# Kernel tuning notes

Measured on AMD Instinct MI355X. Metric: run time of the kernel, lower is better.

## Reference

```python
import jax, jax.numpy as jnp
import numpy as np

DT = 0.001
TAU_INV = 1.0 / 0.006   # tau_mem_inv == tau_syn_inv for both cells
V_TH = 1.0              # norse defaults: v_leak=0, v_reset=0


def heaviside(x):
    return (x > 0).astype(x.dtype)


def setup_inputs() -> dict:
    key = jax.random.key(0)
    k1, k2, k3 = jax.random.split(key, 3)
    T, B, I, H, O = 128, 2048, 64, 256, 16
    inp = jax.random.normal(k1, (T, B, I), dtype=jnp.float32)
    # torch.nn.Linear default init ~ U(-1/sqrt(fan_in), 1/sqrt(fan_in))
    w1 = jax.random.uniform(k2, (H, I), jnp.float32, -1.0, 1.0) / np.sqrt(I)
    w2 = jax.random.uniform(k3, (O, H), jnp.float32, -1.0, 1.0) / np.sqrt(H)
    return {"input": inp, "w1": w1, "w2": w2}


def _snn_forward(inp, w1, w2):
    B = inp.shape[1]
    H, O = w1.shape[0], w2.shape[0]
    decay = 1.0 - DT * TAU_INV

    def step(carry, x_t):
        v1, i1, v2, i2 = carry
        # LIF cell (hidden layer)
        g1 = x_t @ w1.T                              # [B, H]
        v_dec = v1 + DT * TAU_INV * (i1 - v1)        # Euler membrane update
        i_dec = i1 * decay                           # synaptic decay
        z = heaviside(v_dec - V_TH)                  # spikes
        v1n = (1.0 - z) * v_dec                      # reset to 0 where spiked
        i1n = i_dec + g1
        # LI cell (readout)
        g2 = z @ w2.T                                # [B, O]
        v2n = v2 + DT * TAU_INV * (i2 - v2)
        i2n = i2 * decay + g2
        return (v1n, i1n, v2n, i2n), (z, v2n)

    init = (jnp.zeros((B, H), inp.dtype), jnp.zeros((B, H), inp.dtype),
            jnp.zeros((B, O), inp.dtype), jnp.zeros((B, O), inp.dtype))
    _, (zs, ys) = jax.lax.scan(step, init, inp)
    score = jnp.max(ys, axis=0)                      # amax over time -> [B, O]
    spikes_mean = jnp.mean(jnp.sum(zs, axis=(0, 2)))
    return score, spikes_mean


def reference(input, w1, w2):
    return _snn_forward(input, w1, w2)
```

## Files before the change

kernel.cpp:

```cpp
#include <hip/hip_runtime.h>
#include <hip/hip_bf16.h>

#define T_STEPS 128
#define BATCH   2048
#define IN_F    64
#define HID     256
#define OUT_F   16
#define CH      8
#define NCH     (T_STEPS / CH)
#define SLAB    (BATCH * OUT_F)

typedef __attribute__((ext_vector_type(8))) short bf16x8;
typedef __attribute__((ext_vector_type(4))) float f32x4;
typedef unsigned short u16;
typedef unsigned int   u32;

__device__ __forceinline__ u16 f2bf(float f) {
    union { __hip_bfloat16 h; u16 u; } cv;
    cv.h = __float2bfloat16(f);
    return cv.u;
}
__device__ __forceinline__ float bf2f(u16 h) {
    return __uint_as_float(((u32)h) << 16);
}
__device__ __forceinline__ bf16x8 pack8(float4 a, float4 b) {
    bf16x8 r;
    r[0] = (short)f2bf(a.x); r[1] = (short)f2bf(a.y);
    r[2] = (short)f2bf(a.z); r[3] = (short)f2bf(a.w);
    r[4] = (short)f2bf(b.x); r[5] = (short)f2bf(b.y);
    r[6] = (short)f2bf(b.z); r[7] = (short)f2bf(b.w);
    return r;
}

__device__ __forceinline__ void lds_barrier() {
    __builtin_amdgcn_sched_barrier(0);
    asm volatile("s_waitcnt lgkmcnt(0)" ::: "memory");
    __builtin_amdgcn_sched_barrier(0);
    __builtin_amdgcn_s_barrier();
    __builtin_amdgcn_sched_barrier(0);
}

__global__ void snn_init_kernel(float* __restrict__ out) {
    if (threadIdx.x == 0 && blockIdx.x == 0) out[BATCH * OUT_F] = 0.0f;
}

__global__ void __launch_bounds__(512, 2)
snn_l1_kernel(const float* __restrict__ x, const float* __restrict__ w1,
              const float* __restrict__ w2, u16* __restrict__ g2p,
              float* __restrict__ out)
{
    const int tid  = threadIdx.x;
    const int lane = tid & 63;
    const int wv   = tid >> 6;
    const int hi   = lane >> 4;
    const int l15  = lane & 15;
    const int tile = blockIdx.x & 127;
    const int half = blockIdx.x >> 7;
    const int row0 = tile * 16;
    const int hbase = half * 128 + wv * 16;

    __shared__ __attribute__((aligned(16))) u16 xl[2][CH * 2 * 512];
    __shared__ __attribute__((aligned(16))) u16 zb[2][CH * 4 * 512];
    __shared__ float sacc;
    if (tid == 0) sacc = 0.f;

    const f32x4 zf = {0.f, 0.f, 0.f, 0.f};
    const float dt_tau = (float)(0.001 * (1.0 / 0.006));
    const float decay  = (float)(1.0 - 0.001 * (1.0 / 0.006));

    bf16x8 w1f[2];
#pragma unroll
    for (int kh = 0; kh < 2; ++kh) {
        const float* src = &w1[(hbase + l15) * IN_F + kh * 32 + hi * 8];
        w1f[kh] = pack8(*(const float4*)src, *(const float4*)(src + 4));
    }
    bf16x8 w2f[4];
#pragma unroll
    for (int kt = 0; kt < 4; ++kt) {
        const int k0 = half * 128 + kt * 32 + hi * 8;
        w2f[kt] = pack8(*(const float4*)&w2[l15 * HID + k0],
                        *(const float4*)&w2[l15 * HID + k0 + 4]);
    }

    const size_t cstride = (size_t)CH * BATCH * IN_F;
    const float* gp[2];
    int wofs[2];
#pragma unroll
    for (int j = 0; j < 2; ++j) {
        const int u  = tid + 512 * j;
        const int s  = u >> 7, r7 = u & 127;
        const int f  = r7 >> 6, chi = (r7 >> 4) & 3, cl = r7 & 15;
        wofs[j] = (s * 2 + f) * 512 + (chi * 16 + cl) * 8;
        gp[j]   = x + ((size_t)s * BATCH + row0 + cl) * IN_F + f * 32 + chi * 8;
    }
    float4 ra[2], rb[2];
#pragma unroll
    for (int j = 0; j < 2; ++j) {
        ra[j] = *(const float4*)gp[j];
        rb[j] = *(const float4*)(gp[j] + 4);
        *(bf16x8*)&xl[0][wofs[j]] = pack8(ra[j], rb[j]);
    }
#pragma unroll
    for (int j = 0; j < 2; ++j) {
        ra[j] = *(const float4*)(gp[j] + cstride);
        rb[j] = *(const float4*)(gp[j] + cstride + 4);
        gp[j] += 2 * cstride;
    }

    const int zwkey = ((l15 >> 3) << 5) | (((hi >> 1) & 1) << 4);
    const int zwofs = (wv >> 1) * 512
                    + (((((wv & 1) * 2 + (hi >> 1)) * 16 + l15) * 8 + (hi & 1) * 4)
                       ^ zwkey);
    const int zrkey = ((l15 >> 3) << 5) | ((hi & 1) << 4);
    const int zrofs = ((hi * 16 + l15) * 8) ^ zrkey;

    f32x4 v1 = zf, i1 = zf;
    int wcnt = 0;
    lds_barrier();

    for (int c = 0; c < NCH; ++c) {
        const int cb = c & 1;
        const u16* xb = &xl[cb][0];
        u16* zw = &zb[cb][0];

        bf16x8 xfa[CH], xfb[CH];
#pragma unroll
        for (int s = 0; s < 2; ++s) {
            xfa[s] = *(const bf16x8*)&xb[(s * 2 + 0) * 512 + lane * 8];
            xfb[s] = *(const bf16x8*)&xb[(s * 2 + 1) * 512 + lane * 8];
        }
        uint2 zi[CH];
#pragma unroll
        for (int s = 0; s < CH; ++s) {
            if (s + 2 < CH) {
                xfa[s + 2] = *(const bf16x8*)&xb[((s + 2) * 2 + 0) * 512 + lane * 8];
                xfb[s + 2] = *(const bf16x8*)&xb[((s + 2) * 2 + 1) * 512 + lane * 8];
            }
            f32x4 g1 = __builtin_amdgcn_mfma_f32_16x16x32_bf16(w1f[0], xfa[s], zf, 0, 0, 0);
            g1 = __builtin_amdgcn_mfma_f32_16x16x32_bf16(w1f[1], xfb[s], g1, 0, 0, 0);

            const f32x4 vd = v1 + dt_tau * (i1 - v1);
            bool sp[4];
#pragma unroll
            for (int r = 0; r < 4; ++r) {
                sp[r] = vd[r] > 1.0f;
                v1[r] = sp[r] ? 0.f : vd[r];
                wcnt += __popcll(__ballot(sp[r]));
            }
            i1 = i1 * decay + g1;

            zi[s].x = (sp[0] ? 0x3F80u : 0u) | (sp[1] ? 0x3F800000u : 0u);
            zi[s].y = (sp[2] ? 0x3F80u : 0u) | (sp[3] ? 0x3F800000u : 0u);
        }
#pragma unroll
        for (int s = 0; s < CH; ++s)
            *(uint2*)&zw[s * 2048 + zwofs] = zi[s];
        if (c + 1 < NCH) {
#pragma unroll
            for (int j = 0; j < 2; ++j)
                *(bf16x8*)&xl[cb ^ 1][wofs[j]] = pack8(ra[j], rb[j]);
        }

        lds_barrier();

        if (c + 2 < NCH) {
#pragma unroll
            for (int j = 0; j < 2; ++j) {
                ra[j] = *(const float4*)gp[j];
                rb[j] = *(const float4*)(gp[j] + 4);
                gp[j] += cstride;
            }
        }
        {
            const u16* zr = &zb[cb][wv * 2048];
            f32x4 g2 = zf;
#pragma unroll
            for (int kt = 0; kt < 4; ++kt) {
                const bf16x8 zfr = *(const bf16x8*)&zr[kt * 512 + zrofs];
                g2 = __builtin_amdgcn_mfma_f32_16x16x32_bf16(zfr, w2f[kt], g2, 0, 0, 0);
            }
            u16* dst = g2p + (size_t)half * (T_STEPS * SLAB)
                     + (size_t)(c * CH + wv) * SLAB + (row0 + 4 * hi) * OUT_F + l15;
#pragma unroll
            for (int r = 0; r < 4; ++r) dst[r * OUT_F] = f2bf(g2[r]);
        }
    }

    if (lane == 0) atomicAdd(&sacc, (float)wcnt);
    __syncthreads();
    if (tid == 0) atomicAdd(&out[BATCH * OUT_F], sacc * (1.0f / BATCH));
}

__global__ void __launch_bounds__(256)
snn_li_kernel(const u16* __restrict__ g2p, float* __restrict__ out)
{
    const int gid = blockIdx.x * 256 + threadIdx.x;
    const u16* p0 = g2p + gid;
    const u16* p1 = p0 + (size_t)T_STEPS * SLAB;
    const float dt_tau = (float)(0.001 * (1.0 / 0.006));
    const float decay  = (float)(1.0 - 0.001 * (1.0 / 0.006));
    float v2 = 0.f, i2 = 0.f, ymax = -1e30f;
#pragma unroll 8
    for (int t = 0; t < T_STEPS; ++t) {
        const size_t o = (size_t)t * SLAB;
        const float g = bf2f(p0[o]) + bf2f(p1[o]);
        v2 = fmaf(dt_tau, i2 - v2, v2);
        ymax = fmaxf(ymax, v2);
        i2 = i2 * decay + g;
    }
    out[gid] = ymax;
}

extern "C" void kernel_launch(void* const* d_in, const int* in_sizes, int n_in,
                              void* d_out, int out_size, void* d_ws, size_t ws_size,
                              hipStream_t stream) {
    const float* x  = (const float*)d_in[0];
    const float* w1 = (const float*)d_in[1];
    const float* w2 = (const float*)d_in[2];
    float* out = (float*)d_out;
    u16* g2p = (u16*)d_ws;

    hipLaunchKernelGGL(snn_init_kernel, dim3(1), dim3(64), 0, stream, out);
    hipLaunchKernelGGL(snn_l1_kernel, dim3(256), dim3(512), 0, stream,
                       x, w1, w2, g2p, out);
    hipLaunchKernelGGL(snn_li_kernel, dim3(BATCH * OUT_F / 256), dim3(256), 0,
                       stream, g2p, out);
}
```

Baseline: 53.91 us.

## Software-pipeline LIF chunks with readout MMA, interleave waves, drop init kernel

Restructures the per-chunk loop so the LIF update for chunk c+1 (phase A) and the readout MFMA for chunk c (phase C) sit between a single barrier per iteration. Even waves run A first and odd waves run C first, so MFMA and VALU work from different waves can overlap. The LDS prefetch depth rises from 2 to 3 steps, and the readout MFMAs are split into two accumulator chains under raised priority. The spike count now goes to per-wave partials in workspace and is reduced in the LI kernel, which removes the init kernel launch and the atomics, at the cost of extra workspace and a serial reduction in block 0.

```diff
diff --git a/kernel.cpp b/kernel.cpp
--- a/kernel.cpp
+++ b/kernel.cpp
@@ -9,6 +9,7 @@
 #define CH      8
 #define NCH     (T_STEPS / CH)
 #define SLAB    (BATCH * OUT_F)
+#define SPART_OFS (32u * 1024u * 1024u)
 
 typedef __attribute__((ext_vector_type(8))) short bf16x8;
 typedef __attribute__((ext_vector_type(4))) float f32x4;
@@ -40,14 +41,10 @@
     __builtin_amdgcn_sched_barrier(0);
 }
 
-__global__ void snn_init_kernel(float* __restrict__ out) {
-    if (threadIdx.x == 0 && blockIdx.x == 0) out[BATCH * OUT_F] = 0.0f;
-}
-
 __global__ void __launch_bounds__(512, 2)
 snn_l1_kernel(const float* __restrict__ x, const float* __restrict__ w1,
               const float* __restrict__ w2, u16* __restrict__ g2p,
-              float* __restrict__ out)
+              u32* __restrict__ spart)
 {
     const int tid  = threadIdx.x;
     const int lane = tid & 63;
@@ -61,8 +58,6 @@
 
     __shared__ __attribute__((aligned(16))) u16 xl[2][CH * 2 * 512];
     __shared__ __attribute__((aligned(16))) u16 zb[2][CH * 4 * 512];
-    __shared__ float sacc;
-    if (tid == 0) sacc = 0.f;
 
     const f32x4 zf = {0.f, 0.f, 0.f, 0.f};
     const float dt_tau = (float)(0.001 * (1.0 / 0.006));
@@ -116,25 +111,36 @@
 
     f32x4 v1 = zf, i1 = zf;
     int wcnt = 0;
-    lds_barrier();
-
-    for (int c = 0; c < NCH; ++c) {
-        const int cb = c & 1;
-        const u16* xb = &xl[cb][0];
-        u16* zw = &zb[cb][0];
-
+
+    auto phaseA = [&](int k) {
+        const int kb = k & 1;
+        const u16* xb = &xl[kb][0];
+        u16* zw = &zb[kb][0];
+        if (k + 1 < NCH) {
+#pragma unroll
+            for (int j = 0; j < 2; ++j)
+                *(bf16x8*)&xl[kb ^ 1][wofs[j]] = pack8(ra[j], rb[j]);
+        }
+        if (k + 2 < NCH) {
+#pragma unroll
+            for (int j = 0; j < 2; ++j) {
+                ra[j] = *(const float4*)gp[j];
+                rb[j] = *(const float4*)(gp[j] + 4);
+                gp[j] += cstride;
+            }
+        }
         bf16x8 xfa[CH], xfb[CH];
 #pragma unroll
-        for (int s = 0; s < 2; ++s) {
+        for (int s = 0; s < 3; ++s) {
             xfa[s] = *(const bf16x8*)&xb[(s * 2 + 0) * 512 + lane * 8];
             xfb[s] = *(const bf16x8*)&xb[(s * 2 + 1) * 512 + lane * 8];
         }
         uint2 zi[CH];
 #pragma unroll
         for (int s = 0; s < CH; ++s) {
-            if (s + 2 < CH) {
-                xfa[s + 2] = *(const bf16x8*)&xb[((s + 2) * 2 + 0) * 512 + lane * 8];
-                xfb[s + 2] = *(const bf16x8*)&xb[((s + 2) * 2 + 1) * 512 + lane * 8];
+            if (s + 3 < CH) {
+                xfa[s + 3] = *(const bf16x8*)&xb[((s + 3) * 2 + 0) * 512 + lane * 8];
+                xfb[s + 3] = *(const bf16x8*)&xb[((s + 3) * 2 + 1) * 512 + lane * 8];
             }
             f32x4 g1 = __builtin_amdgcn_mfma_f32_16x16x32_bf16(w1f[0], xfa[s], zf, 0, 0, 0);
             g1 = __builtin_amdgcn_mfma_f32_16x16x32_bf16(w1f[1], xfb[s], g1, 0, 0, 0);
@@ -148,51 +154,54 @@
                 wcnt += __popcll(__ballot(sp[r]));
             }
             i1 = i1 * decay + g1;
-
             zi[s].x = (sp[0] ? 0x3F80u : 0u) | (sp[1] ? 0x3F800000u : 0u);
             zi[s].y = (sp[2] ? 0x3F80u : 0u) | (sp[3] ? 0x3F800000u : 0u);
         }
 #pragma unroll
         for (int s = 0; s < CH; ++s)
             *(uint2*)&zw[s * 2048 + zwofs] = zi[s];
-        if (c + 1 < NCH) {
-#pragma unroll
-            for (int j = 0; j < 2; ++j)
-                *(bf16x8*)&xl[cb ^ 1][wofs[j]] = pack8(ra[j], rb[j]);
-        }
-
+    };
+
+    auto phaseC = [&](int c) {
+        const int cb = c & 1;
+        const u16* zr = &zb[cb][wv * 2048];
+        const bf16x8 z0 = *(const bf16x8*)&zr[0 * 512 + zrofs];
+        const bf16x8 z1 = *(const bf16x8*)&zr[1 * 512 + zrofs];
+        const bf16x8 z2 = *(const bf16x8*)&zr[2 * 512 + zrofs];
+        const bf16x8 z3 = *(const bf16x8*)&zr[3 * 512 + zrofs];
+        __builtin_amdgcn_s_setprio(1);
+        f32x4 ga = __builtin_amdgcn_mfma_f32_16x16x32_bf16(z0, w2f[0], zf, 0, 0, 0);
+        f32x4 gb = __builtin_amdgcn_mfma_f32_16x16x32_bf16(z1, w2f[1], zf, 0, 0, 0);
+        ga = __builtin_amdgcn_mfma_f32_16x16x32_bf16(z2, w2f[2], ga, 0, 0, 0);
+        gb = __builtin_amdgcn_mfma_f32_16x16x32_bf16(z3, w2f[3], gb, 0, 0, 0);
+        __builtin_amdgcn_s_setprio(0);
+        const f32x4 g2 = ga + gb;
+        u16* dst = g2p + (size_t)half * (T_STEPS * SLAB)
+                 + (size_t)(c * CH + wv) * SLAB + (row0 + 4 * hi) * OUT_F + l15;
+#pragma unroll
+        for (int r = 0; r < 4; ++r) dst[r * OUT_F] = f2bf(g2[r]);
+    };
+
+    lds_barrier();
+    phaseA(0);
+
+    for (int c = 0; c < NCH; ++c) {
         lds_barrier();
-
-        if (c + 2 < NCH) {
-#pragma unroll
-            for (int j = 0; j < 2; ++j) {
-                ra[j] = *(const float4*)gp[j];
-                rb[j] = *(const float4*)(gp[j] + 4);
-                gp[j] += cstride;
-            }
-        }
-        {
-            const u16* zr = &zb[cb][wv * 2048];
-            f32x4 g2 = zf;
-#pragma unroll
-            for (int kt = 0; kt < 4; ++kt) {
-                const bf16x8 zfr = *(const bf16x8*)&zr[kt * 512 + zrofs];
-                g2 = __builtin_amdgcn_mfma_f32_16x16x32_bf16(zfr, w2f[kt], g2, 0, 0, 0);
-            }
-            u16* dst = g2p + (size_t)half * (T_STEPS * SLAB)
-                     + (size_t)(c * CH + wv) * SLAB + (row0 + 4 * hi) * OUT_F + l15;
-#pragma unroll
-            for (int r = 0; r < 4; ++r) dst[r * OUT_F] = f2bf(g2[r]);
-        }
-    }
-
-    if (lane == 0) atomicAdd(&sacc, (float)wcnt);
-    __syncthreads();
-    if (tid == 0) atomicAdd(&out[BATCH * OUT_F], sacc * (1.0f / BATCH));
+        if ((wv & 1) == 0) {
+            if (c + 1 < NCH) phaseA(c + 1);
+            phaseC(c);
+        } else {
+            phaseC(c);
+            if (c + 1 < NCH) phaseA(c + 1);
+        }
+    }
+
+    if (lane == 0) spart[blockIdx.x * 8 + wv] = (u32)wcnt;
 }
 
 __global__ void __launch_bounds__(256)
-snn_li_kernel(const u16* __restrict__ g2p, float* __restrict__ out)
+snn_li_kernel(const u16* __restrict__ g2p, const u32* __restrict__ spart,
+              float* __restrict__ out)
 {
     const int gid = blockIdx.x * 256 + threadIdx.x;
     const u16* p0 = g2p + gid;
@@ -209,6 +218,20 @@
         i2 = i2 * decay + g;
     }
     out[gid] = ymax;
+
+    if (blockIdx.x == 0) {
+        u32 s = 0;
+#pragma unroll
+        for (int i = 0; i < 8; ++i) s += spart[threadIdx.x * 8 + i];
+#pragma unroll
+        for (int m = 1; m < 64; m <<= 1) s += __shfl_xor(s, m, 64);
+        __shared__ u32 sb[4];
+        if ((threadIdx.x & 63) == 0) sb[threadIdx.x >> 6] = s;
+        __syncthreads();
+        if (threadIdx.x == 0)
+            out[BATCH * OUT_F] =
+                (float)(sb[0] + sb[1] + sb[2] + sb[3]) * (1.0f / BATCH);
+    }
 }
 
 extern "C" void kernel_launch(void* const* d_in, const int* in_sizes, int n_in,
@@ -218,11 +241,11 @@
     const float* w1 = (const float*)d_in[1];
     const float* w2 = (const float*)d_in[2];
     float* out = (float*)d_out;
-    u16* g2p = (u16*)d_ws;
-
-    hipLaunchKernelGGL(snn_init_kernel, dim3(1), dim3(64), 0, stream, out);
+    u16* g2p   = (u16*)d_ws;
+    u32* spart = (u32*)((char*)d_ws + SPART_OFS);
+
     hipLaunchKernelGGL(snn_l1_kernel, dim3(256), dim3(512), 0, stream,
-                       x, w1, w2, g2p, out);
+                       x, w1, w2, g2p, spart);
     hipLaunchKernelGGL(snn_li_kernel, dim3(BATCH * OUT_F / 256), dim3(256), 0,
-                       stream, g2p, out);
-}
+                       stream, g2p, spart, out);
+}
```

Result: faster. 44.55 us (-17.4%).
